# Optimization experiments

Measured on AMD Instinct MI355X. Metric: run time of the kernel, lower is better.

The kernel has to match this reference:

```python
import jax, jax.numpy as jnp
import numpy as np

N, E, B = 40000, 640000, 8192
IN, META, HID, OUT = 768, 6, 256, 128
NE, K, REL, NET = 4, 2, 200, 3
NL, NH, FF = 4, 4, 512


def setup_inputs():
    key = jax.random.key(0)
    keys = iter(jax.random.split(key, 64))
    def p(*shape):
        return jax.random.normal(next(keys), shape, jnp.float32) * 0.02
    return dict(
        x=jax.random.normal(next(keys), (N, IN + META), jnp.float32),
        noise=jax.random.normal(next(keys), (3, B, NE), jnp.float32),
        g_lin1_w=p(HID, IN + META), g_lin1_b=p(HID),
        conv_W=p(2, HID, HID), conv_Wr=p(2, HID, REL), conv_a=p(2, 3 * HID),
        conv_Wres=p(2, HID, HID), conv_rel=p(2, NET, REL),
        g_lin2_w=p(OUT, HID), g_lin2_b=p(OUT),
        te_w=p(OUT, IN), te_b=p(OUT),
        me_w1=p(HID, META), me_b1=p(HID), me_w2=p(OUT, HID), me_b2=p(OUT),
        moe_gate_w=p(3, NE, OUT), moe_noise_w=p(3, OUT),
        moe_w1=p(3, NE, 4 * OUT, OUT), moe_b1=p(3, NE, 4 * OUT),
        moe_w2=p(3, NE, OUT, 4 * OUT), moe_b2=p(3, NE, OUT),
        tf_qkv_w=p(NL, 3 * OUT, OUT), tf_qkv_b=p(NL, 3 * OUT),
        tf_out_w=p(NL, OUT, OUT), tf_out_b=p(NL, OUT),
        tf_ln1_g=jnp.ones((NL, OUT), jnp.float32), tf_ln1_b=jnp.zeros((NL, OUT), jnp.float32),
        tf_ff1_w=p(NL, FF, OUT), tf_ff1_b=p(NL, FF),
        tf_ff2_w=p(NL, OUT, FF), tf_ff2_b=p(NL, OUT),
        tf_ln2_g=jnp.ones((NL, OUT), jnp.float32), tf_ln2_b=jnp.zeros((NL, OUT), jnp.float32),
        clf_w=p(2, 3 * OUT), clf_b=p(2),
        edge_index=jax.random.randint(next(keys), (2, E), 0, N),
        edge_type=jax.random.randint(next(keys), (E,), 0, NET),
        batch_size=B,
    )


def _seg_softmax(logit, seg, n):
    m = jax.ops.segment_max(logit, seg, num_segments=n)
    e = jnp.exp(logit - m[seg])
    s = jax.ops.segment_sum(e, seg, num_segments=n)
    return e / (s[seg] + 1e-16)


def _hgn_layer(h, src, dst, et, W, Wr, a, Wres, rel, final):
    n, d = h.shape[0], W.shape[0]
    Wx = h @ W.T  # [N, HID]
    # a(cat(Wx_i, Wx_j, Wr_rel)) decomposed: per-node + per-edge-type scalars
    s_i = Wx @ a[:d]
    s_j = Wx @ a[d:2 * d]
    r_s = (rel @ Wr.T) @ a[2 * d:]  # [NET]
    logit = jax.nn.leaky_relu(s_i[dst] + s_j[src] + r_s[et], 0.2)
    alpha = _seg_softmax(logit, dst, n)
    agg = jax.ops.segment_sum(Wx[src] * alpha[:, None], dst, num_segments=n)
    out = jax.nn.elu(agg + h @ Wres.T)
    if final:
        out = out / jnp.maximum(jnp.linalg.norm(out, axis=1, keepdims=True), 1e-12)
    return out


def _moe(xv, eps, gate_w, noise_w, w1, b1, w2, b2):
    g = xv @ gate_w.T                       # [B, NE]
    nsd = jax.nn.softplus(xv @ noise_w)     # [B]
    h = g + eps * nsd[:, None]
    _, bot = jax.lax.top_k(-h, K)           # bottom-K experts get -inf
    drop = jnp.sum(jax.nn.one_hot(bot, NE, dtype=h.dtype), axis=1) > 0
    h = jnp.where(drop, -jnp.inf, h)
    L = jax.nn.softmax(h, axis=1)
    logits, idx = jax.lax.top_k(L, K)
    tmp = L.sum(0)
    loss = (jnp.std(tmp, ddof=1) / jnp.mean(tmp)) ** 2
    comb = jnp.einsum('bs,bse->be', logits, jax.nn.one_hot(idx, NE, dtype=L.dtype))
    h1 = jax.nn.relu(jnp.einsum('bd,ehd->ebh', xv, w1) + b1[:, None, :])
    eo = jnp.einsum('ebh,eoh->ebo', h1, w2) + b2[:, None, :]  # [NE, B, OUT]
    return jnp.einsum('be,ebo->bo', comb, eo), loss


def _ln(x, g, b):
    mu = x.mean(-1, keepdims=True)
    var = x.var(-1, keepdims=True)
    return (x - mu) / jnp.sqrt(var + 1e-5) * g + b


def _tf_layer(x, qkv_w, qkv_b, out_w, out_b, ln1g, ln1b, f1w, f1b, f2w, f2b, ln2g, ln2b):
    Bq, S, D = x.shape
    hd = D // NH
    qkv = x @ qkv_w.T + qkv_b
    q, k, v = jnp.split(qkv, 3, axis=-1)
    q = q.reshape(Bq, S, NH, hd)
    k = k.reshape(Bq, S, NH, hd)
    v = v.reshape(Bq, S, NH, hd)
    att = jax.nn.softmax(jnp.einsum('bshd,bthd->bhst', q, k) / jnp.sqrt(jnp.float32(hd)), axis=-1)
    o = jnp.einsum('bhst,bthd->bshd', att, v).reshape(Bq, S, D)
    x = _ln(x + o @ out_w.T + out_b, ln1g, ln1b)
    ff = jax.nn.relu(x @ f1w.T + f1b) @ f2w.T + f2b
    return _ln(x + ff, ln2g, ln2b)


def _forward(x, noise, g_lin1_w, g_lin1_b, conv_W, conv_Wr, conv_a, conv_Wres, conv_rel,
             g_lin2_w, g_lin2_b, te_w, te_b, me_w1, me_b1, me_w2, me_b2,
             moe_gate_w, moe_noise_w, moe_w1, moe_b1, moe_w2, moe_b2,
             tf_qkv_w, tf_qkv_b, tf_out_w, tf_out_b, tf_ln1_g, tf_ln1_b,
             tf_ff1_w, tf_ff1_b, tf_ff2_w, tf_ff2_b, tf_ln2_g, tf_ln2_b,
             clf_w, clf_b, edge_index, edge_type, batch_size):
    src, dst = edge_index[0], edge_index[1]
    # graph encoder (dropout is eval no-op)
    h = jax.nn.relu(x @ g_lin1_w.T + g_lin1_b)
    h = _hgn_layer(h, src, dst, edge_type, conv_W[0], conv_Wr[0], conv_a[0], conv_Wres[0], conv_rel[0], False)
    h = _hgn_layer(h, src, dst, edge_type, conv_W[1], conv_Wr[1], conv_a[1], conv_Wres[1], conv_rel[1], True)
    graph = jax.nn.relu(h @ g_lin2_w.T + g_lin2_b)
    x_g = graph[:batch_size]
    text = x[:batch_size, :IN]
    meta = x[:batch_size, IN:]
    x_t = jax.nn.relu(text @ te_w.T + te_b)
    x_m = jax.nn.relu(jax.nn.relu(meta @ me_w1.T + me_b1) @ me_w2.T + me_b2)
    outs, losses = [], []
    for i, xv in enumerate((x_g, x_t, x_m)):
        o, l = _moe(xv, noise[i], moe_gate_w[i], moe_noise_w[i], moe_w1[i], moe_b1[i], moe_w2[i], moe_b2[i])
        outs.append(o)
        losses.append(l)
    loss = losses[0] + losses[1] + losses[2]
    z = jnp.stack(outs, axis=1)  # [B, 3, OUT]
    for li in range(NL):
        z = _tf_layer(z, tf_qkv_w[li], tf_qkv_b[li], tf_out_w[li], tf_out_b[li],
                      tf_ln1_g[li], tf_ln1_b[li], tf_ff1_w[li], tf_ff1_b[li],
                      tf_ff2_w[li], tf_ff2_b[li], tf_ln2_g[li], tf_ln2_b[li])
    logits = z.reshape(z.shape[0], -1) @ clf_w.T + clf_b
    return logits, loss


def reference(x, noise, g_lin1_w, g_lin1_b, conv_W, conv_Wr, conv_a, conv_Wres, conv_rel,
              g_lin2_w, g_lin2_b, te_w, te_b, me_w1, me_b1, me_w2, me_b2,
              moe_gate_w, moe_noise_w, moe_w1, moe_b1, moe_w2, moe_b2,
              tf_qkv_w, tf_qkv_b, tf_out_w, tf_out_b, tf_ln1_g, tf_ln1_b,
              tf_ff1_w, tf_ff1_b, tf_ff2_w, tf_ff2_b, tf_ln2_g, tf_ln2_b,
              clf_w, clf_b, edge_index, edge_type, batch_size):
    return _forward(x, noise, g_lin1_w, g_lin1_b, conv_W, conv_Wr, conv_a, conv_Wres, conv_rel,
                    g_lin2_w, g_lin2_b, te_w, te_b, me_w1, me_b1, me_w2, me_b2,
                    moe_gate_w, moe_noise_w, moe_w1, moe_b1, moe_w2, moe_b2,
                    tf_qkv_w, tf_qkv_b, tf_out_w, tf_out_b, tf_ln1_g, tf_ln1_b,
                    tf_ff1_w, tf_ff1_b, tf_ff2_w, tf_ff2_b, tf_ln2_g, tf_ln2_b,
                    clf_w, clf_b, edge_index, edge_type, batch_size)
```

## Files before the change

kernel.cpp:

```cpp
#include <hip/hip_runtime.h>
#include <hip/hip_bf16.h>
#include <math.h>

#define NN 40000
#define EE 640000
#define BB 8192
#define IN_DIM 768
#define META_DIM 6
#define XDIM 774
#define HID 256
#define OUT_D 128
#define NEXP 4
#define NET_T 3
#define REL_D 200
#define NLAY 4
#define FF_D 512

typedef __attribute__((ext_vector_type(8))) short short8;
typedef __attribute__((ext_vector_type(4))) float f32x4;

__device__ __forceinline__ ushort f2bf(float f) {
    union { float f; unsigned u; } a; a.f = f;
    unsigned u = a.u;
    unsigned r = (u + 0x7FFFu + ((u >> 16) & 1u)) >> 16;
// ... 275 lines not shown
            *(short8*)&Ash[row * 40 + c8 * 8] = hi;
            *(short8*)&Asl[row * 40 + c8 * 8] = lo;
        }
        {
            int row = t >> 2, c8 = t & 3;
            short8 hi, lo;
            if (B_PACKED) {
                unsigned u[8] = {bpk[0].x, bpk[0].y, bpk[0].z, bpk[0].w,
                                 bpk[1].x, bpk[1].y, bpk[1].z, bpk[1].w};
#pragma unroll
                for (int e = 0; e < 8; e++) { hi[e] = (short)(u[e] >> 16); lo[e] = (short)(u[e] & 0xFFFFu); }
            } else {
                float f[8] = {bfp[0].x, bfp[0].y, bfp[0].z, bfp[0].w,
                              bfp[1].x, bfp[1].y, bfp[1].z, bfp[1].w};
#pragma unroll
                for (int e = 0; e < 8; e++) {
                    ushort h = f2bf(f[e]);
                    hi[e] = (short)h;
                    lo[e] = (short)f2bf(f[e] - bf2f(h));
                }
            }
            *(short8*)&Bsh[row * 40 + c8 * 8] = hi;
            *(short8*)&Bsl[row * 40 + c8 * 8] = lo;
        }
    };

    f32x4 acc[WM][2];
#pragma unroll
    for (int i = 0; i < WM; i++)
#pragma unroll
        for (int j = 0; j < 2; j++) acc[i][j] = (f32x4){0.f, 0.f, 0.f, 0.f};

    loadA(0); loadB(0);
    for (int k0 = 0; k0 < K; k0 += 32) {
        storeTiles();
        __syncthreads();
        if (k0 + 32 < K) { loadA(k0 + 32); loadB(k0 + 32); }

        short8 ah[WM], al[WM];
#pragma unroll
        for (int i = 0; i < WM; i++) {
            int ro = (wm * (WM * 16) + i * 16 + r) * 40 + quad * 8;
            ah[i] = *(const short8*)&Ash[ro];
            al[i] = *(const short8*)&Asl[ro];
        }
#pragma unroll
        for (int j = 0; j < 2; j++) {
            int ro = (wn * 32 + j * 16 + r) * 40 + quad * 8;
            short8 bh = *(const short8*)&Bsh[ro];
            short8 bl = *(const short8*)&Bsl[ro];
#pragma unroll
            for (int i = 0; i < WM; i++)
                acc[i][j] = __builtin_amdgcn_mfma_f32_16x16x32_bf16(ah[i], bh, acc[i][j], 0, 0, 0);
#pragma unroll
            for (int i = 0; i < WM; i++)
                acc[i][j] = __builtin_amdgcn_mfma_f32_16x16x32_bf16(ah[i], bl, acc[i][j], 0, 0, 0);
#pragma unroll
            for (int i = 0; i < WM; i++)
                acc[i][j] = __builtin_amdgcn_mfma_f32_16x16x32_bf16(al[i], bh, acc[i][j], 0, 0, 0);
        }
        __syncthreads();
    }

#pragma unroll
    for (int j = 0; j < 2; j++) {
        int col = bn + wn * 32 + j * 16 + r;
        float bc = bias ? bias[col] : 0.f;
#pragma unroll
        for (int i = 0; i < WM; i++) {
#pragma unroll
            for (int reg = 0; reg < 4; reg++) {
                int row = bm + wm * (WM * 16) + i * 16 + quad * 4 + reg;
                if (row >= M) continue;
                float v = acc[i][j][reg] + bc;
                if (HAS_RES) v += res[(size_t)row * Nn + col];
                if (ACT == 1) v = fmaxf(v, 0.f);
                else if (ACT == 2) v = (v > 0.f) ? v : expm1f(v);
                if (OUT_SPLIT) Cpk[(size_t)row * Nn + col] = packsplit(v);
                else           C[(size_t)row * Nn + col] = v;
            }
        }
    }
}

template<int WM, int ACT, int HAS_RES, int OUT_SPLIT, int A_FP32, int B_PACKED>
static void m3_launch(const void* Ap, int lda, int Kreal, const void* Bp, int ldb,
                      const float* bias, const float* res,
                      float* C, unsigned* Cpk,
                      int M, int Nn, int K, hipStream_t s)
{
    const int BM = 32 * WM;
    dim3 grid(Nn / 64, (M + BM - 1) / BM);
    mfma3k<WM, ACT, HAS_RES, OUT_SPLIT, A_FP32, B_PACKED><<<grid, 256, 0, s>>>(
        Ap, lda, Kreal, Bp, ldb, bias, res, C, Cpk, M, Nn, K);
}

template<int ACT>
__global__ void gemm_kernel(const float* __restrict__ A, int lda,
                            const float* __restrict__ Bw,
                            const float* __restrict__ bias,
                            const float* __restrict__ res,
                            float* __restrict__ C, int M, int Nn, int K)
{
    __shared__ float As[16][68];
    __shared__ float Bs[16][68];
    int bm = blockIdx.y * 64, bn = blockIdx.x * 64;
    int t = threadIdx.x;
    int tx = t & 15, ty = t >> 4;
    float acc[4][4] = {{0.f}};

    for (int k0 = 0; k0 < K; k0 += 16) {
#pragma unroll
        for (int i = 0; i < 4; i++) {
            int l = t * 4 + i; int mm = l >> 4, kk = l & 15;
            int gm = bm + mm, gk = k0 + kk;
            As[kk][mm] = (gm < M && gk < K) ? A[(size_t)gm * lda + gk] : 0.f;
        }
#pragma unroll
        for (int i = 0; i < 4; i++) {
            int l = t * 4 + i; int nn = l >> 4, kk = l & 15;
            int gn = bn + nn, gk = k0 + kk;
            Bs[kk][nn] = (gn < Nn && gk < K) ? Bw[(size_t)gn * K + gk] : 0.f;
        }
        __syncthreads();
#pragma unroll
        for (int kk = 0; kk < 16; kk++) {
            float4 a4 = *reinterpret_cast<const float4*>(&As[kk][ty * 4]);
            float4 b4 = *reinterpret_cast<const float4*>(&Bs[kk][tx * 4]);
            float a0[4] = {a4.x, a4.y, a4.z, a4.w};
            float b0[4] = {b4.x, b4.y, b4.z, b4.w};
#pragma unroll
            for (int i = 0; i < 4; i++)
#pragma unroll
                for (int j = 0; j < 4; j++)
                    acc[i][j] += a0[i] * b0[j];
        }
        __syncthreads();
    }
#pragma unroll
    for (int i = 0; i < 4; i++) {
        int gm = bm + ty * 4 + i; if (gm >= M) continue;
#pragma unroll
        for (int j = 0; j < 4; j++) {
            int gn = bn + tx * 4 + j; if (gn >= Nn) continue;
            float v = acc[i][j];
            if (bias) v += bias[gn];
            if (res)  v += res[(size_t)gm * Nn + gn];
            if (ACT == 1) v = fmaxf(v, 0.f);
            C[(size_t)gm * Nn + gn] = v;
        }
    }
}

template<int ACT, int A_BF16, int OUT_BF16>
__global__ __launch_bounds__(256) void mfma_gemm(
    const void* __restrict__ Ap, size_t strideAz,
    const float* __restrict__ Bw, size_t strideBz,
    const float* __restrict__ bias, size_t strideBiasz,
    void* __restrict__ Cp, size_t strideCz,
    int M, int Nn, int K)
{
    __shared__ __align__(16) ushort As[64 * 40];
    __shared__ __align__(16) ushort Bs[64 * 40];

    int z = blockIdx.z;
    const float*  Af  = (const float*)Ap  + (A_BF16 ? 0 : z * strideAz);
    const ushort* Ab  = (const ushort*)Ap + (A_BF16 ? z * strideAz : 0);
    const float*  Bwz = Bw + z * strideBz;
    const float*  bz  = bias ? bias + z * strideBiasz : nullptr;
    float*  Cf = (float*)Cp  + (OUT_BF16 ? 0 : z * strideCz);
    ushort* Cb = (ushort*)Cp + (OUT_BF16 ? z * strideCz : 0);

    int bn = blockIdx.x * 64;
    int bm = blockIdx.y * 64;
    int t = threadIdx.x;
    int wave = t >> 6, lane = t & 63;
    int wm = wave & 1, wn = wave >> 1;
    int quad = lane >> 4, r = lane & 15;

    short8 apre_b;
    float4 apre_f[2];
    float4 bpre[2];
    int ar = t >> 2, ac = t & 3;

    auto loadA = [&](int k0) {
        if (A_BF16) {
            apre_b = *(const short8*)(Ab + (size_t)(bm + ar) * K + k0 + ac * 8);
        } else {
#pragma unroll
            for (int i = 0; i < 2; i++) {
                int idx = t + i * 256;
                int row = idx >> 3, c4 = idx & 7;
                apre_f[i] = *(const float4*)(Af + (size_t)(bm + row) * K + k0 + c4 * 4);
            }
        }
    };
    auto loadB = [&](int k0) {
        const float* p = Bwz + (size_t)(bn + ar) * K + k0 + ac * 8;
        bpre[0] = *(const float4*)p;
        bpre[1] = *(const float4*)(p + 4);
    };
    auto storeTiles = [&]() {
        if (A_BF16) {
            *(short8*)&As[ar * 40 + ac * 8] = apre_b;
        } else {
#pragma unroll
            for (int i = 0; i < 2; i++) {
                int idx = t + i * 256;
                int row = idx >> 3, c4 = idx & 7;
                ushort4 u;
                u.x = f2bf(apre_f[i].x); u.y = f2bf(apre_f[i].y);
                u.z = f2bf(apre_f[i].z); u.w = f2bf(apre_f[i].w);
                *(ushort4*)&As[row * 40 + c4 * 4] = u;
            }
        }
        {
            float f[8] = {bpre[0].x, bpre[0].y, bpre[0].z, bpre[0].w,
                          bpre[1].x, bpre[1].y, bpre[1].z, bpre[1].w};
            short8 hb;
#pragma unroll
            for (int e = 0; e < 8; e++) hb[e] = (short)f2bf(f[e]);
            *(short8*)&Bs[ar * 40 + ac * 8] = hb;
        }
    };

    f32x4 acc[2][2];
#pragma unroll
    for (int i = 0; i < 2; i++)
#pragma unroll
        for (int j = 0; j < 2; j++) acc[i][j] = (f32x4){0.f, 0.f, 0.f, 0.f};

    loadA(0); loadB(0);
    for (int k0 = 0; k0 < K; k0 += 32) {
        storeTiles();
        __syncthreads();
        if (k0 + 32 < K) { loadA(k0 + 32); loadB(k0 + 32); }

        short8 af[2];
#pragma unroll
        for (int i = 0; i < 2; i++)
            af[i] = *(const short8*)&As[(wm * 32 + i * 16 + r) * 40 + quad * 8];
#pragma unroll
        for (int j = 0; j < 2; j++) {
            short8 bf = *(const short8*)&Bs[(wn * 32 + j * 16 + r) * 40 + quad * 8];
#pragma unroll
            for (int i = 0; i < 2; i++)
                acc[i][j] = __builtin_amdgcn_mfma_f32_16x16x32_bf16(af[i], bf, acc[i][j], 0, 0, 0);
        }
        __syncthreads();
    }

#pragma unroll
    for (int j = 0; j < 2; j++) {
        int col = bn + wn * 32 + j * 16 + r;
        float bc = bz ? bz[col] : 0.f;
#pragma unroll
        for (int i = 0; i < 2; i++) {
#pragma unroll
            for (int reg = 0; reg < 4; reg++) {
                int row = bm + wm * 32 + i * 16 + quad * 4 + reg;
                float v = acc[i][j][reg] + bc;
                if (ACT == 1) v = fmaxf(v, 0.f);
                if (OUT_BF16) Cb[(size_t)row * Nn + col] = f2bf(v);
                else          Cf[(size_t)row * Nn + col] = v;
            }
        }
    }
}

template<int ACT, int A_BF16, int OUT_BF16>
static void mfma_launch(const void* A, size_t sAz, const float* Bw, size_t sBz,
                        const float* bias, size_t sbz, void* C, size_t sCz,
                        int M, int Nn, int K, int batch, hipStream_t s)
{
    dim3 grid(Nn / 64, M / 64, batch);
    mfma_gemm<ACT, A_BF16, OUT_BF16><<<grid, 256, 0, s>>>(A, sAz, Bw, sBz, bias, sbz, C, sCz, M, Nn, K);
}

__global__ void sisj_kernel(const float* __restrict__ Wx, const float* __restrict__ a,
                            float* __restrict__ s_i, float* __restrict__ s_j, int n)
{
    int t = threadIdx.x; int w = t >> 6, l = t & 63;
    int m = blockIdx.x * 4 + w; if (m >= n) return;
    const float* r = Wx + (size_t)m * HID;
    float v1 = 0.f, v2 = 0.f;
#pragma unroll
    for (int i = 0; i < 4; i++) {
        float xv = r[l + 64 * i];
        v1 += xv * a[l + 64 * i];
        v2 += xv * a[HID + l + 64 * i];
    }
    for (int off = 32; off; off >>= 1) { v1 += __shfl_down(v1, off); v2 += __shfl_down(v2, off); }
    if (l == 0) { s_i[m] = v1; s_j[m] = v2; }
}

__global__ void rs_kernel(const float* __restrict__ Wr, const float* __restrict__ rel,
                          const float* __restrict__ a3, float* __restrict__ rs)
{
    __shared__ float red[256];
    int tt = blockIdx.x; int j = threadIdx.x;
    const float* relr = rel + tt * REL_D;
    const float* wr = Wr + (size_t)j * REL_D;
    float wsum = 0.f;
    for (int k = 0; k < REL_D; k++) wsum += wr[k] * relr[k];
    red[j] = wsum * a3[j];
    __syncthreads();
    for (int s2 = 128; s2; s2 >>= 1) { if (j < s2) red[j] += red[j + s2]; __syncthreads(); }
    if (j == 0) rs[tt] = red[0];
}

__global__ void deg_kernel(const int* __restrict__ dst, int* __restrict__ deg)
{
    int e = blockIdx.x * blockDim.x + threadIdx.x;
    if (e < EE) atomicAdd(&deg[dst[e]], 1);
}

__global__ void scan_kernel(const int* __restrict__ deg, int* __restrict__ rowstart,
                            int* __restrict__ cursor, int n)
{
    __shared__ int bs[1024];
    int t = threadIdx.x;
    int base = t * 40;
    int loc[40];
    int sum = 0;
#pragma unroll
    for (int i = 0; i < 40; i++) {
        int v = (base + i < n) ? deg[base + i] : 0;
        loc[i] = sum; sum += v;
    }
    bs[t] = sum;
    __syncthreads();
    for (int off = 1; off < 1024; off <<= 1) {
        int x = (t >= off) ? bs[t - off] : 0;
        __syncthreads();
        bs[t] += x;
        __syncthreads();
    }
    int excl = bs[t] - sum;
#pragma unroll
    for (int i = 0; i < 40; i++) {
        if (base + i < n) { int v = excl + loc[i]; rowstart[base + i] = v; cursor[base + i] = v; }
    }
    if (t == 1023) rowstart[n] = bs[1023];
}

__global__ void fill_kernel(const int* __restrict__ src, const int* __restrict__ dst,
                            const int* __restrict__ et, int* __restrict__ cursor,
                            unsigned* __restrict__ csr_val)
{
    int e = blockIdx.x * blockDim.x + threadIdx.x;
    if (e >= EE) return;
    int d = dst[e];
    int pos = atomicAdd(&cursor[d], 1);
    csr_val[pos] = (unsigned)src[e] | ((unsigned)et[e] << 16);
}

__global__ void csr_agg_kernel(const unsigned* __restrict__ csr_val,
                               const int* __restrict__ rowstart,
                               const float* __restrict__ s_i, const float* __restrict__ s_j,
                               const float* __restrict__ rsv,
                               const float* __restrict__ Wx, float* __restrict__ agg,
                               int nlim)
{
    int t = threadIdx.x; int w = t >> 6, l = t & 63;
    int node = blockIdx.x * 4 + w; if (node >= nlim) return;
    int start = rowstart[node], end = rowstart[node + 1];
    float r0 = rsv[0], r1 = rsv[1], r2 = rsv[2];
    float si = s_i[node];

    float m = -INFINITY;
    for (int i = start + l; i < end; i += 64) {
        unsigned v = csr_val[i];
        int s = v & 0xFFFF; int et = v >> 16;
        float rr = (et == 0) ? r0 : ((et == 1) ? r1 : r2);
        float lg = si + s_j[s] + rr;
        lg = (lg >= 0.f) ? lg : 0.2f * lg;
        m = fmaxf(m, lg);
    }
    for (int off = 32; off; off >>= 1) m = fmaxf(m, __shfl_down(m, off));
    m = __shfl(m, 0);

    float a0 = 0.f, a1 = 0.f, a2 = 0.f, a3 = 0.f, ssum = 0.f;
    for (int c = start; c < end; c += 64) {
        int nchunk = min(64, end - c);
        float wgt = 0.f; int sidx = 0;
        if (l < nchunk) {
            unsigned v = csr_val[c + l];
            sidx = v & 0xFFFF; int et = v >> 16;
            float rr = (et == 0) ? r0 : ((et == 1) ? r1 : r2);
            float lg = si + s_j[sidx] + rr;
            lg = (lg >= 0.f) ? lg : 0.2f * lg;
            wgt = expf(lg - m);
            ssum += wgt;
        }
        int j = 0;
        for (; j + 4 <= nchunk; j += 4) {
            float w0 = __shfl(wgt, j),     w1 = __shfl(wgt, j + 1);
            float w2 = __shfl(wgt, j + 2), w3 = __shfl(wgt, j + 3);
            int s0 = __shfl(sidx, j),     s1 = __shfl(sidx, j + 1);
            int s2 = __shfl(sidx, j + 2), s3 = __shfl(sidx, j + 3);
            const float* p0 = Wx + (size_t)s0 * HID + l;
            const float* p1 = Wx + (size_t)s1 * HID + l;
            const float* p2 = Wx + (size_t)s2 * HID + l;
            const float* p3 = Wx + (size_t)s3 * HID + l;
            float v00 = p0[0], v01 = p0[64], v02 = p0[128], v03 = p0[192];
            float v10 = p1[0], v11 = p1[64], v12 = p1[128], v13 = p1[192];
            float v20 = p2[0], v21 = p2[64], v22 = p2[128], v23 = p2[192];
            float v30 = p3[0], v31 = p3[64], v32 = p3[128], v33 = p3[192];
            a0 += w0 * v00 + w1 * v10 + w2 * v20 + w3 * v30;
            a1 += w0 * v01 + w1 * v11 + w2 * v21 + w3 * v31;
            a2 += w0 * v02 + w1 * v12 + w2 * v22 + w3 * v32;
            a3 += w0 * v03 + w1 * v13 + w2 * v23 + w3 * v33;
        }
        for (; j < nchunk; j++) {
            float wj = __shfl(wgt, j);
            int sj = __shfl(sidx, j);
            const float* wr = Wx + (size_t)sj * HID + l;
            a0 += wj * wr[0];
            a1 += wj * wr[64];
            a2 += wj * wr[128];
            a3 += wj * wr[192];
        }
    }
    for (int off = 32; off; off >>= 1) ssum += __shfl_down(ssum, off);
    ssum = __shfl(ssum, 0);
    float inv = 1.f / (ssum + 1e-16f);
    float* ar = agg + (size_t)node * HID;
    ar[l] = a0 * inv; ar[l + 64] = a1 * inv; ar[l + 128] = a2 * inv; ar[l + 192] = a3 * inv;
}

__global__ void rownorm_pack(unsigned* __restrict__ pk, int n)
{
    int t = threadIdx.x; int w = t >> 6, l = t & 63;
    int m = blockIdx.x * 4 + w; if (m >= n) return;
    size_t base = (size_t)m * HID;
    float vals[4]; float q = 0.f;
#pragma unroll
    for (int i = 0; i < 4; i++) {
        unsigned u = pk[base + l + 64 * i];
        vals[i] = bf2f((ushort)(u >> 16)) + bf2f((ushort)(u & 0xFFFFu));
        q += vals[i] * vals[i];
    }
    for (int off = 32; off; off >>= 1) q += __shfl_down(q, off);
    q = __shfl(q, 0);
    float inv = 1.f / fmaxf(sqrtf(q), 1e-12f);
#pragma unroll
    for (int i = 0; i < 4; i++)
        pk[base + l + 64 * i] = packsplit(vals[i] * inv);
}

__global__ void moe_gate_kernel(const float* __restrict__ xv, const float* __restrict__ gate_w,
                                const float* __restrict__ noise_w, const float* __restrict__ eps,
                                float* __restrict__ comb, float* __restrict__ tmpsum)
{
    __shared__ float part[4];
    int t = threadIdx.x; int w = t >> 6, l = t & 63;
    if (t < 4) part[t] = 0.f;
    __syncthreads();
    int b = blockIdx.x * 4 + w;
    const float* xr = xv + (size_t)b * OUT_D;
    float x0 = xr[l], x1 = xr[l + 64];
    float dots[5];
#pragma unroll
    for (int e = 0; e < 4; e++) {
        const float* gw = gate_w + e * OUT_D;
        float v = x0 * gw[l] + x1 * gw[l + 64];
        for (int off = 32; off; off >>= 1) v += __shfl_down(v, off);
        dots[e] = v;
    }
    {
        float v = x0 * noise_w[l] + x1 * noise_w[l + 64];
        for (int off = 32; off; off >>= 1) v += __shfl_down(v, off);
        dots[4] = v;
    }
    if (l == 0) {
        float xg = dots[4];
        float nsd = (xg > 20.f) ? xg : log1pf(expf(xg));
        float hv[4];
#pragma unroll
        for (int e = 0; e < 4; e++) hv[e] = dots[e] + eps[(size_t)b * 4 + e] * nsd;
        int i1 = 0;
        for (int e = 1; e < 4; e++) if (hv[e] < hv[i1]) i1 = e;
        int i2 = -1;
        for (int e = 0; e < 4; e++) { if (e == i1) continue; if (i2 < 0 || hv[e] < hv[i2]) i2 = e; }
        int k1 = -1, k2 = -1;
        for (int e = 0; e < 4; e++) { if (e != i1 && e != i2) { if (k1 < 0) k1 = e; else k2 = e; } }
        float mm = fmaxf(hv[k1], hv[k2]);
        float e1 = expf(hv[k1] - mm), e2 = expf(hv[k2] - mm);
        float s = e1 + e2;
        float L[4] = {0.f, 0.f, 0.f, 0.f};
        L[k1] = e1 / s; L[k2] = e2 / s;
#pragma unroll
        for (int e = 0; e < 4; e++) comb[(size_t)b * 4 + e] = L[e];
        atomicAdd(&part[k1], L[k1]);
        atomicAdd(&part[k2], L[k2]);
    }
    __syncthreads();
    if (t < 4) atomicAdd(&tmpsum[t], part[t]);
}

__global__ void moe_combine_kernel(const float* __restrict__ eo, const float* __restrict__ comb,
                                   float* __restrict__ zout)
{
    int idx = blockIdx.x * blockDim.x + threadIdx.x;
    if (idx >= BB * OUT_D) return;
    int b = idx >> 7, o = idx & 127;
    const size_t S = (size_t)BB * OUT_D;
    float v = comb[b * 4 + 0] * eo[idx] + comb[b * 4 + 1] * eo[idx + S]
            + comb[b * 4 + 2] * eo[idx + 2 * S] + comb[b * 4 + 3] * eo[idx + 3 * S];
    zout[(size_t)b * (3 * OUT_D) + o] = v;
}

__global__ void loss_kernel(const float* __restrict__ tmpsum, float* __restrict__ out)
{
    if (threadIdx.x == 0 && blockIdx.x == 0) {
        float total = 0.f;
        for (int v = 0; v < 3; v++) {
            const float* tp = tmpsum + v * 4;
            float mean = (tp[0] + tp[1] + tp[2] + tp[3]) * 0.25f;
            float var = 0.f;
            for (int e = 0; e < 4; e++) { float d = tp[e] - mean; var += d * d; }
            var /= 3.f;
            float r = sqrtf(var) / mean;
            total += r * r;
        }
        out[0] = total;
    }
}

__global__ void attn_kernel(const float* __restrict__ qkv, float* __restrict__ o)
{
    int t = threadIdx.x;
    int half = t >> 5;
    int d = t & 31;
    int task = blockIdx.x * 8 + half;
    int b = task >> 2, h = task & 3;
    const float* base = qkv + (size_t)b * 3 * 384 + h * 32;
    float q0 = base[d],       q1 = base[384 + d],       q2 = base[768 + d];
    float k0 = base[128 + d], k1 = base[384 + 128 + d], k2 = base[768 + 128 + d];
    float v0 = base[256 + d], v1 = base[384 + 256 + d], v2 = base[768 + 256 + d];
    float s[3][3];
    s[0][0] = q0 * k0; s[0][1] = q0 * k1; s[0][2] = q0 * k2;
    s[1][0] = q1 * k0; s[1][1] = q1 * k1; s[1][2] = q1 * k2;
    s[2][0] = q2 * k0; s[2][1] = q2 * k1; s[2][2] = q2 * k2;
#pragma unroll
    for (int i = 0; i < 3; i++)
#pragma unroll
        for (int j = 0; j < 3; j++) {
            float v = s[i][j];
            for (int off = 16; off; off >>= 1) v += __shfl_xor(v, off, 32);
            s[i][j] = v;
        }
    const float scale = 0.17677669529663687f;
    float outv[3];
#pragma unroll
    for (int i = 0; i < 3; i++) {
        float a0 = s[i][0] * scale, a1 = s[i][1] * scale, a2 = s[i][2] * scale;
        float m = fmaxf(a0, fmaxf(a1, a2));
        float e0 = expf(a0 - m), e1 = expf(a1 - m), e2 = expf(a2 - m);
        float inv = 1.f / (e0 + e1 + e2);
        outv[i] = (e0 * v0 + e1 * v1 + e2 * v2) * inv;
    }
    float* ob = o + (size_t)b * 3 * 128 + h * 32;
    ob[d] = outv[0]; ob[128 + d] = outv[1]; ob[256 + d] = outv[2];
}

__global__ void ln_residual_kernel(float* __restrict__ x, const float* __restrict__ add,
                                   const float* __restrict__ g, const float* __restrict__ bta, int M)
{
    int t = threadIdx.x; int w = t >> 6, l = t & 63;
    int row = blockIdx.x * 4 + w; if (row >= M) return;
    float* xr = x + (size_t)row * 128;
    const float* ar = add + (size_t)row * 128;
    float v0 = xr[l] + ar[l], v1 = xr[l + 64] + ar[l + 64];
    float s = v0 + v1;
    for (int off = 32; off; off >>= 1) s += __shfl_down(s, off);
    s = __shfl(s, 0);
    float mu = s * (1.f / 128.f);
    float d0 = v0 - mu, d1 = v1 - mu;
    float q = d0 * d0 + d1 * d1;
    for (int off = 32; off; off >>= 1) q += __shfl_down(q, off);
    q = __shfl(q, 0);
    float inv = rsqrtf(q * (1.f / 128.f) + 1e-5f);
    xr[l]      = d0 * inv * g[l] + bta[l];
    xr[l + 64] = d1 * inv * g[l + 64] + bta[l + 64];
}

__global__ void clf_kernel(const float* __restrict__ z, const float* __restrict__ w,
                           const float* __restrict__ b, float* __restrict__ out)
{
    int t = threadIdx.x; int wv = t >> 6, l = t & 63;
    int row = blockIdx.x * 4 + wv; if (row >= BB) return;
    const float* zr = z + (size_t)row * 384;
    float v0 = 0.f, v1 = 0.f;
    for (int i = l; i < 384; i += 64) {
        float zz = zr[i];
        v0 += zz * w[i];
        v1 += zz * w[384 + i];
    }
    for (int off = 32; off; off >>= 1) { v0 += __shfl_down(v0, off); v1 += __shfl_down(v1, off); }
    if (l == 0) { out[row * 2] = v0 + b[0]; out[row * 2 + 1] = v1 + b[1]; }
}

extern "C" void kernel_launch(void* const* d_in, const int* in_sizes, int n_in,
                              void* d_out, int out_size, void* d_ws, size_t ws_size,
                              hipStream_t stream)
{
    const float* x         = (const float*)d_in[0];
    const float* noise     = (const float*)d_in[1];
    const float* g_lin1_w  = (const float*)d_in[2];
    const float* g_lin1_b  = (const float*)d_in[3];
    const float* conv_W    = (const float*)d_in[4];
    const float* conv_Wr   = (const float*)d_in[5];
    const float* conv_a    = (const float*)d_in[6];
    const float* conv_Wres = (const float*)d_in[7];
    const float* conv_rel  = (const float*)d_in[8];
    const float* g_lin2_w  = (const float*)d_in[9];
    const float* g_lin2_b  = (const float*)d_in[10];
    const float* te_w      = (const float*)d_in[11];
    const float* te_b      = (const float*)d_in[12];
    const float* me_w1     = (const float*)d_in[13];
    const float* me_b1     = (const float*)d_in[14];
    const float* me_w2     = (const float*)d_in[15];
    const float* me_b2     = (const float*)d_in[16];
    const float* moe_gate_w  = (const float*)d_in[17];
    const float* moe_noise_w = (const float*)d_in[18];
    const float* moe_w1    = (const float*)d_in[19];
    const float* moe_b1    = (const float*)d_in[20];
    const float* moe_w2    = (const float*)d_in[21];
    const float* moe_b2    = (const float*)d_in[22];
    const float* tf_qkv_w  = (const float*)d_in[23];
    const float* tf_qkv_b  = (const float*)d_in[24];
    const float* tf_out_w  = (const float*)d_in[25];
    const float* tf_out_b  = (const float*)d_in[26];
    const float* tf_ln1_g  = (const float*)d_in[27];
    const float* tf_ln1_b  = (const float*)d_in[28];
    const float* tf_ff1_w  = (const float*)d_in[29];
    const float* tf_ff1_b  = (const float*)d_in[30];
    const float* tf_ff2_w  = (const float*)d_in[31];
    const float* tf_ff2_b  = (const float*)d_in[32];
    const float* tf_ln2_g  = (const float*)d_in[33];
    const float* tf_ln2_b  = (const float*)d_in[34];
    const float* clf_w     = (const float*)d_in[35];
    const float* clf_b     = (const float*)d_in[36];
    const int*   edge_index = (const int*)d_in[37];
    const int*   edge_type  = (const int*)d_in[38];

    float* ws = (float*)d_ws;

    const size_t F_A = 0;
    const size_t F_B = 10240000;
    const size_t F_C = 22822912;
    const size_t F_D = 33062912;
    const size_t F_M = 43302912;
    const size_t F_X = 44200000;

    unsigned* hApk = (unsigned*)(ws + F_A);
    float* qkv    = ws + F_A;
    float* wx     = ws + F_B;
    float* graph  = ws + F_B;
    ushort* ff1bf = (ushort*)(ws + F_B);
    float* agg    = ws + F_C;
    float* x_mh   = ws + F_C;
    ushort* h1bf  = (ushort*)(ws + F_C);
    float* attn_o = ws + F_C;
    float* tmp1   = ws + F_C + 3200000;
    unsigned* hBpk = (unsigned*)(ws + F_D);
    float* z      = ws + F_D;
    float* x_t    = ws + F_D + 3200000;
    float* x_m    = ws + F_D + 4300000;
    float* eo     = ws + F_D + 5400000;

    float* s_i    = ws + F_M;
    float* s_j    = ws + F_M + 40000;
    float* rsv    = ws + F_M + 80000;
    float* comb   = ws + F_M + 80016;
    float* tmpsum = ws + F_M + 112784;
    int* deg      = (int*)(ws + F_M + 120000);
    int* rowstart = (int*)(ws + F_M + 161000);
    int* cursor   = (int*)(ws + F_M + 202000);
    unsigned* csr_val = (unsigned*)(ws + F_M + 242000);

    unsigned* xpk  = (unsigned*)(ws + F_X);
    unsigned* wpk  = (unsigned*)(ws + F_X + 32000000);

    const int* srcv = edge_index;
    const int* dstv = edge_index + EE;

    hipMemsetAsync(deg, 0, NN * sizeof(int), stream);
    deg_kernel<<<(EE + 255) / 256, 256, 0, stream>>>(dstv, deg);
    scan_kernel<<<1, 1024, 0, stream>>>(deg, rowstart, cursor, NN);
    fill_kernel<<<(EE + 255) / 256, 256, 0, stream>>>(srcv, dstv, edge_type, cursor, csr_val);

    cvt_pack(x, XDIM, XDIM, xpk, NN, 800, stream);
    cvt_pack(g_lin1_w, XDIM, XDIM, wpk, HID, 800, stream);
    m128_launch<1, 0, 1, 1>(xpk, 800, wpk, 800, g_lin1_b, nullptr,
                            nullptr, hApk, NN, HID, 800, stream);

    unsigned *inpk = hApk, *outpk = hBpk;
    for (int layer = 0; layer < 2; layer++) {
        const float* W    = conv_W    + (size_t)layer * HID * HID;
        const float* Wr   = conv_Wr   + (size_t)layer * HID * REL_D;
        const float* a    = conv_a    + (size_t)layer * 3 * HID;
        const float* Wres = conv_Wres + (size_t)layer * HID * HID;
        const float* rel  = conv_rel  + (size_t)layer * NET_T * REL_D;
        int mOut = (layer == 1) ? BB : NN;

        m128_launch<0, 0, 0, 0>(inpk, HID, W, HID, nullptr, nullptr,
                                wx, nullptr, NN, HID, HID, stream);
        sisj_kernel<<<NN / 4, 256, 0, stream>>>(wx, a, s_i, s_j, NN);
        rs_kernel<<<NET_T, 256, 0, stream>>>(Wr, rel, a + 2 * HID, rsv);
        csr_agg_kernel<<<(mOut + 3) / 4, 256, 0, stream>>>(csr_val, rowstart, s_i, s_j, rsv, wx, agg, mOut);
        if (layer == 0)
            m128_launch<2, 1, 1, 0>(inpk, HID, Wres, HID, nullptr, agg,
                                    nullptr, outpk, mOut, HID, HID, stream);
        else
            m3_launch<2, 2, 1, 1, 0, 0>(inpk, HID, HID, Wres, HID, nullptr, agg,
                                        nullptr, outpk, mOut, HID, HID, stream);
        unsigned* tp = inpk; inpk = outpk; outpk = tp;
    }
    rownorm_pack<<<BB / 4, 256, 0, stream>>>(inpk, BB);

    m3_launch<2, 1, 0, 0, 0, 0>(inpk, HID, HID, g_lin2_w, HID, g_lin2_b, nullptr,
                                graph, nullptr, BB, OUT_D, HID, stream);

    m3_launch<2, 1, 0, 0, 0, 0>(xpk, 800, IN_DIM, te_w, IN_DIM, te_b, nullptr,
                                x_t, nullptr, BB, OUT_D, IN_DIM, stream);
    {
        dim3 g((HID + 63) / 64, (BB + 63) / 64);
        gemm_kernel<1><<<g, 256, 0, stream>>>(x + IN_DIM, XDIM, me_w1, me_b1, nullptr,
                                              x_mh, BB, HID, META_DIM);
    }
    m3_launch<2, 1, 0, 0, 1, 0>(x_mh, HID, HID, me_w2, HID, me_b2, nullptr,
                                x_m, nullptr, BB, OUT_D, HID, stream);

    hipMemsetAsync(tmpsum, 0, 16 * sizeof(float), stream);
    const float* xvs[3] = { graph, x_t, x_m };
    for (int v = 0; v < 3; v++) {
        const float* xv = xvs[v];
        moe_gate_kernel<<<BB / 4, 256, 0, stream>>>(
            xv, moe_gate_w + (size_t)v * NEXP * OUT_D, moe_noise_w + (size_t)v * OUT_D,
            noise + (size_t)v * BB * NEXP, comb, tmpsum + v * 4);
        mfma_launch<1, 0, 1>(xv, 0,
                             moe_w1 + (size_t)v * 4 * FF_D * OUT_D, (size_t)FF_D * OUT_D,
                             moe_b1 + (size_t)v * 4 * FF_D, FF_D,
                             h1bf, (size_t)BB * FF_D,
                             BB, FF_D, OUT_D, 4, stream);
        mfma_launch<0, 1, 0>(h1bf, (size_t)BB * FF_D,
                             moe_w2 + (size_t)v * 4 * OUT_D * FF_D, (size_t)OUT_D * FF_D,
                             moe_b2 + (size_t)v * 4 * OUT_D, OUT_D,
                             eo, (size_t)BB * OUT_D,
                             BB, OUT_D, FF_D, 4, stream);
        moe_combine_kernel<<<(BB * OUT_D) / 256, 256, 0, stream>>>(eo, comb, z + v * OUT_D);
    }

    const int MT = BB * 3;
    for (int li = 0; li < NLAY; li++) {
        mfma_launch<0, 0, 0>(z, 0, tf_qkv_w + (size_t)li * 384 * 128, 0,
                             tf_qkv_b + li * 384, 0, qkv, 0, MT, 384, 128, 1, stream);
        attn_kernel<<<(BB * 4) / 8, 256, 0, stream>>>(qkv, attn_o);
        mfma_launch<0, 0, 0>(attn_o, 0, tf_out_w + (size_t)li * 128 * 128, 0,
                             tf_out_b + li * 128, 0, tmp1, 0, MT, 128, 128, 1, stream);
        ln_residual_kernel<<<MT / 4, 256, 0, stream>>>(z, tmp1, tf_ln1_g + li * 128, tf_ln1_b + li * 128, MT);
        mfma_launch<1, 0, 1>(z, 0, tf_ff1_w + (size_t)li * 512 * 128, 0,
                             tf_ff1_b + li * 512, 0, ff1bf, 0, MT, 512, 128, 1, stream);
        mfma_launch<0, 1, 0>(ff1bf, 0, tf_ff2_w + (size_t)li * 128 * 512, 0,
                             tf_ff2_b + li * 128, 0, tmp1, 0, MT, 128, 512, 1, stream);
        ln_residual_kernel<<<MT / 4, 256, 0, stream>>>(z, tmp1, tf_ln2_g + li * 128, tf_ln2_b + li * 128, MT);
    }

    clf_kernel<<<BB / 4, 256, 0, stream>>>(z, clf_w, clf_b, (float*)d_out);
    loss_kernel<<<1, 64, 0, stream>>>(tmpsum, (float*)d_out + BB * 2);
}
```

Baseline: 1.544 ms.

## Fuse MoE combine into expert GEMMs and LayerNorm into transformer GEMMs

```diff
diff --git a/kernel.cpp b/kernel.cpp
--- a/kernel.cpp
+++ b/kernel.cpp
@@ -451,12 +451,13 @@
     }
 }
 
-template<int ACT, int A_BF16, int OUT_BF16>
+template<int ACT, int A_BF16, int OUT_BF16, int SCALE>
 __global__ __launch_bounds__(256) void mfma_gemm(
     const void* __restrict__ Ap, size_t strideAz,
     const float* __restrict__ Bw, size_t strideBz,
     const float* __restrict__ bias, size_t strideBiasz,
     void* __restrict__ Cp, size_t strideCz,
+    const float* __restrict__ combp,
     int M, int Nn, int K)
 {
     __shared__ __align__(16) ushort As[64 * 40];
@@ -560,6 +561,7 @@
                 int row = bm + wm * 32 + i * 16 + quad * 4 + reg;
                 float v = acc[i][j][reg] + bc;
                 if (ACT == 1) v = fmaxf(v, 0.f);
+                if (SCALE) v *= combp[(size_t)row * 4 + (z & 3)];
                 if (OUT_BF16) Cb[(size_t)row * Nn + col] = f2bf(v);
                 else          Cf[(size_t)row * Nn + col] = v;
             }
@@ -567,13 +569,248 @@
     }
 }
 
-template<int ACT, int A_BF16, int OUT_BF16>
+template<int ACT, int A_BF16, int OUT_BF16, int SCALE>
 static void mfma_launch(const void* A, size_t sAz, const float* Bw, size_t sBz,
                         const float* bias, size_t sbz, void* C, size_t sCz,
+                        const float* combp,
                         int M, int Nn, int K, int batch, hipStream_t s)
 {
     dim3 grid(Nn / 64, M / 64, batch);
-    mfma_gemm<ACT, A_BF16, OUT_BF16><<<grid, 256, 0, s>>>(A, sAz, Bw, sBz, bias, sbz, C, sCz, M, Nn, K);
+    mfma_gemm<ACT, A_BF16, OUT_BF16, SCALE><<<grid, 256, 0, s>>>(
+        A, sAz, Bw, sBz, bias, sbz, C, sCz, combp, M, Nn, K);
+}
+
+__global__ __launch_bounds__(256) void moe_w2s_kernel(
+    const ushort* __restrict__ h1, const float* __restrict__ w2v,
+    const float* __restrict__ b2v, const float* __restrict__ combv,
+    float* __restrict__ zout)
+{
+    __shared__ __align__(16) ushort As[64 * 40];
+    __shared__ __align__(16) ushort Bs[128 * 40];
+
+    int bm = blockIdx.x * 64;
+    int t = threadIdx.x;
+    int wave = t >> 6, lane = t & 63;
+    int wm = wave & 1, wn = wave >> 1;
+    int quad = lane >> 4, r = lane & 15;
+
+    short8 apre;
+    float4 bpre[2][2];
+    int ar = t >> 2, ac = t & 3;
+
+    auto loadA = [&](int k0) {
+        int e = k0 >> 9, j0 = k0 & 511;
+        apre = *(const short8*)(h1 + ((size_t)e * BB + bm + ar) * FF_D + j0 + ac * 8);
+    };
+    auto loadB = [&](int k0) {
+        int e = k0 >> 9, j0 = k0 & 511;
+#pragma unroll
+        for (int i = 0; i < 2; i++) {
+            int idx = t + i * 256;
+            int row = idx >> 2, c8 = idx & 3;
+            const float* p = w2v + ((size_t)e * OUT_D + row) * FF_D + j0 + c8 * 8;
+            bpre[i][0] = *(const float4*)p;
+            bpre[i][1] = *(const float4*)(p + 4);
+        }
+    };
+    auto storeTiles = [&]() {
+        *(short8*)&As[ar * 40 + ac * 8] = apre;
+#pragma unroll
+        for (int i = 0; i < 2; i++) {
+            int idx = t + i * 256;
+            int row = idx >> 2, c8 = idx & 3;
+            float f[8] = {bpre[i][0].x, bpre[i][0].y, bpre[i][0].z, bpre[i][0].w,
+                          bpre[i][1].x, bpre[i][1].y, bpre[i][1].z, bpre[i][1].w};
+            short8 hb;
+#pragma unroll
+            for (int e = 0; e < 8; e++) hb[e] = (short)f2bf(f[e]);
+            *(short8*)&Bs[row * 40 + c8 * 8] = hb;
+        }
+    };
+
+    f32x4 acc[2][4];
+#pragma unroll
+    for (int i = 0; i < 2; i++)
+#pragma unroll
+        for (int j = 0; j < 4; j++) acc[i][j] = (f32x4){0.f, 0.f, 0.f, 0.f};
+
+    loadA(0); loadB(0);
+    for (int k0 = 0; k0 < 4 * FF_D; k0 += 32) {
+        storeTiles();
+        __syncthreads();
+        if (k0 + 32 < 4 * FF_D) { loadA(k0 + 32); loadB(k0 + 32); }
+
+        short8 af[2];
+#pragma unroll
+        for (int i = 0; i < 2; i++)
+            af[i] = *(const short8*)&As[(wm * 32 + i * 16 + r) * 40 + quad * 8];
+#pragma unroll
+        for (int j = 0; j < 4; j++) {
+            short8 bf = *(const short8*)&Bs[(wn * 64 + j * 16 + r) * 40 + quad * 8];
+#pragma unroll
+            for (int i = 0; i < 2; i++)
+                acc[i][j] = __builtin_amdgcn_mfma_f32_16x16x32_bf16(af[i], bf, acc[i][j], 0, 0, 0);
+        }
+        __syncthreads();
+    }
+
+#pragma unroll
+    for (int j = 0; j < 4; j++) {
+        int col = wn * 64 + j * 16 + r;
+        float b20 = b2v[col], b21 = b2v[OUT_D + col];
+        float b22 = b2v[2 * OUT_D + col], b23 = b2v[3 * OUT_D + col];
+#pragma unroll
+        for (int i = 0; i < 2; i++) {
+#pragma unroll
+            for (int reg = 0; reg < 4; reg++) {
+                int row = bm + wm * 32 + i * 16 + quad * 4 + reg;
+                const float* cb = combv + (size_t)row * 4;
+                float v = acc[i][j][reg]
+                        + cb[0] * b20 + cb[1] * b21 + cb[2] * b22 + cb[3] * b23;
+                zout[(size_t)row * 384 + col] = v;
+            }
+        }
+    }
+}
+
+template<int A_BF16>
+__global__ __launch_bounds__(256) void gemm_ln_kernel(
+    const void* __restrict__ Ap, const float* __restrict__ Bw,
+    const float* __restrict__ bias,
+    float* __restrict__ zio,
+    const float* __restrict__ g, const float* __restrict__ beta,
+    int K)
+{
+    __shared__ __align__(16) ushort As[64 * 40];
+    __shared__ __align__(16) ushort Bs[128 * 40];
+    __shared__ float Cs[64 * 132];
+
+    const float*  Af = (const float*)Ap;
+    const ushort* Ab = (const ushort*)Ap;
+
+    int bm = blockIdx.x * 64;
+    int t = threadIdx.x;
+    int wave = t >> 6, lane = t & 63;
+    int wm = wave & 1, wn = wave >> 1;
+    int quad = lane >> 4, r = lane & 15;
+
+    short8 apre_b;
+    float4 apre_f[2];
+    float4 bpre[2][2];
+    int ar = t >> 2, ac = t & 3;
+
+    auto loadA = [&](int k0) {
+        if (A_BF16) {
+            apre_b = *(const short8*)(Ab + (size_t)(bm + ar) * K + k0 + ac * 8);
+        } else {
+#pragma unroll
+            for (int i = 0; i < 2; i++) {
+                int idx = t + i * 256;
+                int row = idx >> 3, c4 = idx & 7;
+                apre_f[i] = *(const float4*)(Af + (size_t)(bm + row) * K + k0 + c4 * 4);
+            }
+        }
+    };
+    auto loadB = [&](int k0) {
+#pragma unroll
+        for (int i = 0; i < 2; i++) {
+            int idx = t + i * 256;
+            int row = idx >> 2, c8 = idx & 3;
+            const float* p = Bw + (size_t)row * K + k0 + c8 * 8;
+            bpre[i][0] = *(const float4*)p;
+            bpre[i][1] = *(const float4*)(p + 4);
+        }
+    };
+    auto storeTiles = [&]() {
+        if (A_BF16) {
+            *(short8*)&As[ar * 40 + ac * 8] = apre_b;
+        } else {
+#pragma unroll
+            for (int i = 0; i < 2; i++) {
+                int idx = t + i * 256;
+                int row = idx >> 3, c4 = idx & 7;
+                ushort4 u;
+                u.x = f2bf(apre_f[i].x); u.y = f2bf(apre_f[i].y);
+                u.z = f2bf(apre_f[i].z); u.w = f2bf(apre_f[i].w);
+                *(ushort4*)&As[row * 40 + c4 * 4] = u;
+            }
+        }
+#pragma unroll
+        for (int i = 0; i < 2; i++) {
+            int idx = t + i * 256;
+            int row = idx >> 2, c8 = idx & 3;
+            float f[8] = {bpre[i][0].x, bpre[i][0].y, bpre[i][0].z, bpre[i][0].w,
+                          bpre[i][1].x, bpre[i][1].y, bpre[i][1].z, bpre[i][1].w};
+            short8 hb;
+#pragma unroll
+            for (int e = 0; e < 8; e++) hb[e] = (short)f2bf(f[e]);
+            *(short8*)&Bs[row * 40 + c8 * 8] = hb;
+        }
+    };
+
+    f32x4 acc[2][4];
+#pragma unroll
+    for (int i = 0; i < 2; i++)
+#pragma unroll
+        for (int j = 0; j < 4; j++) acc[i][j] = (f32x4){0.f, 0.f, 0.f, 0.f};
+
+    loadA(0); loadB(0);
+    for (int k0 = 0; k0 < K; k0 += 32) {
+        storeTiles();
+        __syncthreads();
+        if (k0 + 32 < K) { loadA(k0 + 32); loadB(k0 + 32); }
+
+        short8 af[2];
+#pragma unroll
+        for (int i = 0; i < 2; i++)
+            af[i] = *(const short8*)&As[(wm * 32 + i * 16 + r) * 40 + quad * 8];
+#pragma unroll
+        for (int j = 0; j < 4; j++) {
+            short8 bf = *(const short8*)&Bs[(wn * 64 + j * 16 + r) * 40 + quad * 8];
+#pragma unroll
+            for (int i = 0; i < 2; i++)
+                acc[i][j] = __builtin_amdgcn_mfma_f32_16x16x32_bf16(af[i], bf, acc[i][j], 0, 0, 0);
+        }
+        __syncthreads();
+    }
+
+#pragma unroll
+    for (int j = 0; j < 4; j++) {
+        int col = wn * 64 + j * 16 + r;
+        float bc = bias[col];
+#pragma unroll
+        for (int i = 0; i < 2; i++) {
+#pragma unroll
+            for (int reg = 0; reg < 4; reg++) {
+                int lrow = wm * 32 + i * 16 + quad * 4 + reg;
+                float y = acc[i][j][reg] + bc + zio[(size_t)(bm + lrow) * 128 + col];
+                Cs[lrow * 132 + col] = y;
+            }
+        }
+    }
+    __syncthreads();
+
+    {
+        int lrow = t >> 2, part = t & 3;
+        const float* rowp = Cs + lrow * 132;
+        float s = 0.f, sq = 0.f;
+#pragma unroll
+        for (int c = 0; c < 32; c++) {
+            float y = rowp[part * 32 + c];
+            s += y; sq += y * y;
+        }
+        s  += __shfl_xor(s, 1);  s  += __shfl_xor(s, 2);
+        sq += __shfl_xor(sq, 1); sq += __shfl_xor(sq, 2);
+        float mu = s * (1.f / 128.f);
+        float var = sq * (1.f / 128.f) - mu * mu;
+        float inv = rsqrtf(var + 1e-5f);
+        float* outp = zio + (size_t)(bm + lrow) * 128 + part * 32;
+#pragma unroll
+        for (int c = 0; c < 32; c++) {
+            int col = part * 32 + c;
+            outp[c] = (rowp[col] - mu) * inv * g[col] + beta[col];
+        }
+    }
 }
 
 __global__ void sisj_kernel(const float* __restrict__ Wx, const float* __restrict__ a,
@@ -748,36 +985,43 @@
         pk[base + l + 64 * i] = packsplit(vals[i] * inv);
 }
 
-__global__ void moe_gate_kernel(const float* __restrict__ xv, const float* __restrict__ gate_w,
-                                const float* __restrict__ noise_w, const float* __restrict__ eps,
-                                float* __restrict__ comb, float* __restrict__ tmpsum)
+__global__ void moe_gate3_kernel(const float* __restrict__ xg, const float* __restrict__ xt,
+                                 const float* __restrict__ xm,
+                                 const float* __restrict__ gate_w, const float* __restrict__ noise_w,
+                                 const float* __restrict__ eps,
+                                 float* __restrict__ comb3, float* __restrict__ tmpsum)
 {
     __shared__ float part[4];
     int t = threadIdx.x; int w = t >> 6, l = t & 63;
     if (t < 4) part[t] = 0.f;
     __syncthreads();
-    int b = blockIdx.x * 4 + w;
+    int gidx = blockIdx.x * 4 + w;
+    int v = gidx / BB, b = gidx % BB;
+    const float* xv = (v == 0) ? xg : (v == 1) ? xt : xm;
+    const float* gw_v = gate_w + (size_t)v * NEXP * OUT_D;
+    const float* nw_v = noise_w + (size_t)v * OUT_D;
     const float* xr = xv + (size_t)b * OUT_D;
     float x0 = xr[l], x1 = xr[l + 64];
     float dots[5];
 #pragma unroll
     for (int e = 0; e < 4; e++) {
-        const float* gw = gate_w + e * OUT_D;
-        float v = x0 * gw[l] + x1 * gw[l + 64];
-        for (int off = 32; off; off >>= 1) v += __shfl_down(v, off);
-        dots[e] = v;
+        const float* gw = gw_v + e * OUT_D;
+        float val = x0 * gw[l] + x1 * gw[l + 64];
+        for (int off = 32; off; off >>= 1) val += __shfl_down(val, off);
+        dots[e] = val;
     }
     {
-        float v = x0 * noise_w[l] + x1 * noise_w[l + 64];
-        for (int off = 32; off; off >>= 1) v += __shfl_down(v, off);
-        dots[4] = v;
+        float val = x0 * nw_v[l] + x1 * nw_v[l + 64];
+        for (int off = 32; off; off >>= 1) val += __shfl_down(val, off);
+        dots[4] = val;
     }
     if (l == 0) {
-        float xg = dots[4];
-        float nsd = (xg > 20.f) ? xg : log1pf(expf(xg));
+        float xgt = dots[4];
+        float nsd = (xgt > 20.f) ? xgt : log1pf(expf(xgt));
         float hv[4];
 #pragma unroll
-        for (int e = 0; e < 4; e++) hv[e] = dots[e] + eps[(size_t)b * 4 + e] * nsd;
+        for (int e = 0; e < 4; e++)
+            hv[e] = dots[e] + eps[((size_t)v * BB + b) * 4 + e] * nsd;
         int i1 = 0;
         for (int e = 1; e < 4; e++) if (hv[e] < hv[i1]) i1 = e;
         int i2 = -1;
@@ -790,24 +1034,12 @@
         float L[4] = {0.f, 0.f, 0.f, 0.f};
         L[k1] = e1 / s; L[k2] = e2 / s;
 #pragma unroll
-        for (int e = 0; e < 4; e++) comb[(size_t)b * 4 + e] = L[e];
+        for (int e = 0; e < 4; e++) comb3[((size_t)v * BB + b) * 4 + e] = L[e];
         atomicAdd(&part[k1], L[k1]);
         atomicAdd(&part[k2], L[k2]);
     }
     __syncthreads();
-    if (t < 4) atomicAdd(&tmpsum[t], part[t]);
-}
-
-__global__ void moe_combine_kernel(const float* __restrict__ eo, const float* __restrict__ comb,
-                                   float* __restrict__ zout)
-{
-    int idx = blockIdx.x * blockDim.x + threadIdx.x;
-    if (idx >= BB * OUT_D) return;
-    int b = idx >> 7, o = idx & 127;
-    const size_t S = (size_t)BB * OUT_D;
-    float v = comb[b * 4 + 0] * eo[idx] + comb[b * 4 + 1] * eo[idx + S]
-            + comb[b * 4 + 2] * eo[idx + 2 * S] + comb[b * 4 + 3] * eo[idx + 3 * S];
-    zout[(size_t)b * (3 * OUT_D) + o] = v;
+    if (t < 4) atomicAdd(&tmpsum[v * 4 + t], part[t]);
 }
 
 __global__ void loss_kernel(const float* __restrict__ tmpsum, float* __restrict__ out)
@@ -862,27 +1094,6 @@
     }
     float* ob = o + (size_t)b * 3 * 128 + h * 32;
     ob[d] = outv[0]; ob[128 + d] = outv[1]; ob[256 + d] = outv[2];
-}
-
-__global__ void ln_residual_kernel(float* __restrict__ x, const float* __restrict__ add,
-                                   const float* __restrict__ g, const float* __restrict__ bta, int M)
-{
-    int t = threadIdx.x; int w = t >> 6, l = t & 63;
-    int row = blockIdx.x * 4 + w; if (row >= M) return;
-    float* xr = x + (size_t)row * 128;
-    const float* ar = add + (size_t)row * 128;
-    float v0 = xr[l] + ar[l], v1 = xr[l + 64] + ar[l + 64];
-    float s = v0 + v1;
-    for (int off = 32; off; off >>= 1) s += __shfl_down(s, off);
-    s = __shfl(s, 0);
-    float mu = s * (1.f / 128.f);
-    float d0 = v0 - mu, d1 = v1 - mu;
-    float q = d0 * d0 + d1 * d1;
-    for (int off = 32; off; off >>= 1) q += __shfl_down(q, off);
-    q = __shfl(q, 0);
-    float inv = rsqrtf(q * (1.f / 128.f) + 1e-5f);
-    xr[l]      = d0 * inv * g[l] + bta[l];
-    xr[l + 64] = d1 * inv * g[l + 64] + bta[l + 64];
 }
 
 __global__ void clf_kernel(const float* __restrict__ z, const float* __restrict__ w,
@@ -963,18 +1174,16 @@
     float* x_mh   = ws + F_C;
     ushort* h1bf  = (ushort*)(ws + F_C);
     float* attn_o = ws + F_C;
-    float* tmp1   = ws + F_C + 3200000;
     unsigned* hBpk = (unsigned*)(ws + F_D);
     float* z      = ws + F_D;
     float* x_t    = ws + F_D + 3200000;
     float* x_m    = ws + F_D + 4300000;
-    float* eo     = ws + F_D + 5400000;
+    float* comb3  = ws + F_D + 5400000;
 
     float* s_i    = ws + F_M;
     float* s_j    = ws + F_M + 40000;
     float* rsv    = ws + F_M + 80000;
-    float* comb   = ws + F_M + 80016;
-    float* tmpsum = ws + F_M + 112784;
+    float* tmpsum = ws + F_M + 80016;
     int* deg      = (int*)(ws + F_M + 120000);
     int* rowstart = (int*)(ws + F_M + 161000);
     int* cursor   = (int*)(ws + F_M + 202000);
@@ -1034,38 +1243,37 @@
                                 x_m, nullptr, BB, OUT_D, HID, stream);
 
     hipMemsetAsync(tmpsum, 0, 16 * sizeof(float), stream);
+    moe_gate3_kernel<<<(3 * BB) / 4, 256, 0, stream>>>(
+        graph, x_t, x_m, moe_gate_w, moe_noise_w, noise, comb3, tmpsum);
     const float* xvs[3] = { graph, x_t, x_m };
     for (int v = 0; v < 3; v++) {
         const float* xv = xvs[v];
-        moe_gate_kernel<<<BB / 4, 256, 0, stream>>>(
-            xv, moe_gate_w + (size_t)v * NEXP * OUT_D, moe_noise_w + (size_t)v * OUT_D,
-            noise + (size_t)v * BB * NEXP, comb, tmpsum + v * 4);
-        mfma_launch<1, 0, 1>(xv, 0,
-                             moe_w1 + (size_t)v * 4 * FF_D * OUT_D, (size_t)FF_D * OUT_D,
-                             moe_b1 + (size_t)v * 4 * FF_D, FF_D,
-                             h1bf, (size_t)BB * FF_D,
-                             BB, FF_D, OUT_D, 4, stream);
-        mfma_launch<0, 1, 0>(h1bf, (size_t)BB * FF_D,
-                             moe_w2 + (size_t)v * 4 * OUT_D * FF_D, (size_t)OUT_D * FF_D,
-                             moe_b2 + (size_t)v * 4 * OUT_D, OUT_D,
-                             eo, (size_t)BB * OUT_D,
-                             BB, OUT_D, FF_D, 4, stream);
-        moe_combine_kernel<<<(BB * OUT_D) / 256, 256, 0, stream>>>(eo, comb, z + v * OUT_D);
+        const float* combv = comb3 + (size_t)v * BB * 4;
+        mfma_launch<1, 0, 1, 1>(xv, 0,
+                                moe_w1 + (size_t)v * 4 * FF_D * OUT_D, (size_t)FF_D * OUT_D,
+                                moe_b1 + (size_t)v * 4 * FF_D, FF_D,
+                                h1bf, (size_t)BB * FF_D, combv,
+                                BB, FF_D, OUT_D, 4, stream);
+        moe_w2s_kernel<<<BB / 64, 256, 0, stream>>>(
+            h1bf, moe_w2 + (size_t)v * 4 * OUT_D * FF_D,
+            moe_b2 + (size_t)v * 4 * OUT_D, combv, z + v * OUT_D);
     }
 
     const int MT = BB * 3;
     for (int li = 0; li < NLAY; li++) {
-        mfma_launch<0, 0, 0>(z, 0, tf_qkv_w + (size_t)li * 384 * 128, 0,
-                             tf_qkv_b + li * 384, 0, qkv, 0, MT, 384, 128, 1, stream);
+        mfma_launch<0, 0, 0, 0>(z, 0, tf_qkv_w + (size_t)li * 384 * 128, 0,
+                                tf_qkv_b + li * 384, 0, qkv, 0, nullptr,
+                                MT, 384, 128, 1, stream);
         attn_kernel<<<(BB * 4) / 8, 256, 0, stream>>>(qkv, attn_o);
-        mfma_launch<0, 0, 0>(attn_o, 0, tf_out_w + (size_t)li * 128 * 128, 0,
-                             tf_out_b + li * 128, 0, tmp1, 0, MT, 128, 128, 1, stream);
-        ln_residual_kernel<<<MT / 4, 256, 0, stream>>>(z, tmp1, tf_ln1_g + li * 128, tf_ln1_b + li * 128, MT);
-        mfma_launch<1, 0, 1>(z, 0, tf_ff1_w + (size_t)li * 512 * 128, 0,
-                             tf_ff1_b + li * 512, 0, ff1bf, 0, MT, 512, 128, 1, stream);
-        mfma_launch<0, 1, 0>(ff1bf, 0, tf_ff2_w + (size_t)li * 128 * 512, 0,
-                             tf_ff2_b + li * 128, 0, tmp1, 0, MT, 128, 512, 1, stream);
-        ln_residual_kernel<<<MT / 4, 256, 0, stream>>>(z, tmp1, tf_ln2_g + li * 128, tf_ln2_b + li * 128, MT);
+        gemm_ln_kernel<0><<<MT / 64, 256, 0, stream>>>(
+            attn_o, tf_out_w + (size_t)li * 128 * 128, tf_out_b + li * 128,
+            z, tf_ln1_g + li * 128, tf_ln1_b + li * 128, 128);
+        mfma_launch<1, 0, 1, 0>(z, 0, tf_ff1_w + (size_t)li * 512 * 128, 0,
+                                tf_ff1_b + li * 512, 0, ff1bf, 0, nullptr,
+                                MT, 512, 128, 1, stream);
+        gemm_ln_kernel<1><<<MT / 64, 256, 0, stream>>>(
+            ff1bf, tf_ff2_w + (size_t)li * 128 * 512, tf_ff2_b + li * 128,
+            z, tf_ln2_g + li * 128, tf_ln2_b + li * 128, 512);
     }
 
     clf_kernel<<<BB / 4, 256, 0, stream>>>(z, clf_w, clf_b, (float*)d_out);
```

Result: slower. 1.626 ms (+5.3%).
